# Optimization experiments

Hardware: AMD Instinct MI355X
Metric: run time of the kernel (lower is better)

The kernel has to match this reference:

```python
import jax, jax.numpy as jnp
import numpy as np
import math

STATE_SIZE = 2048
N_TRIPLES = 16_777_216  # number of indexed triples contracted into the scalar sum


def setup_inputs() -> dict:
    key = jax.random.key(0)
    k_in, k_w, k_idx, k_idx_bw = jax.random.split(key, 4)
    stdv = 1.0 / math.sqrt(STATE_SIZE)
    # state vector
    inp = jax.random.normal(k_in, (STATE_SIZE,), dtype=jnp.float32)
    # nn.Parameter(torch.Tensor(3 * state_size ** 2)) with uniform(-stdv, stdv) init
    weights = jax.random.uniform(
        k_w, (3 * STATE_SIZE * STATE_SIZE,), dtype=jnp.float32,
        minval=-stdv, maxval=stdv)
    # triple index list: col 0 indexes weights, cols 1 and 2 index input.
    # indices in [0, STATE_SIZE) are valid for both tensors.
    idxs = jax.random.randint(k_idx, (N_TRIPLES, 3), 0, STATE_SIZE, dtype=jnp.int32)
    # backward bookkeeping indices (inverse lists for the custom CUDA backward);
    # they do not affect the forward math.
    idxs_bw = jax.random.randint(k_idx_bw, (N_TRIPLES, 3), 0, STATE_SIZE, dtype=jnp.int32)
    return {"input": inp, "weights": weights, "idxs": idxs, "idxs_bw": idxs_bw}


def reference(input, weights, idxs, idxs_bw):
    # Indexed tri-linear weighted contraction:
    #   out = sum_m weights[idxs[m,0]] * input[idxs[m,1]] * input[idxs[m,2]]
    w = jnp.take(weights, idxs[:, 0], axis=0)   # [M]
    a = jnp.take(input, idxs[:, 1], axis=0)     # [M]
    b = jnp.take(input, idxs[:, 2], axis=0)     # [M]
    out = jnp.sum(w * a * b)
    return out[None]  # kernel returns outputs[:1] -> shape [1]
```

## Files before the change

kernel.cpp:

```cpp
#include <hip/hip_runtime.h>

#define STATE 2048
#define BLOCK 256
#define GRID  2048

__global__ void trisum_zero_ws(double* __restrict__ ws) {
    if (blockIdx.x == 0 && threadIdx.x == 0) ws[0] = 0.0;
}

__global__ __launch_bounds__(BLOCK) void trisum_main(
        const float* __restrict__ input,
        const float* __restrict__ weights,
        const int4*  __restrict__ idxs4,
        int ngroups,
        double* __restrict__ ws) {
    __shared__ float s_in[STATE];
    __shared__ float s_w[STATE];
    for (int i = threadIdx.x; i < STATE; i += BLOCK) {
        s_in[i] = input[i];
        s_w[i]  = weights[i];
    }
    __syncthreads();

    float acc = 0.0f;
    const int stride = gridDim.x * blockDim.x;
    for (int g = blockIdx.x * blockDim.x + threadIdx.x; g < ngroups; g += stride) {
        const int4 v0 = idxs4[3 * g + 0];
        const int4 v1 = idxs4[3 * g + 1];
        const int4 v2 = idxs4[3 * g + 2];
        acc += s_w[v0.x] * s_in[v0.y] * s_in[v0.z];
        acc += s_w[v0.w] * s_in[v1.x] * s_in[v1.y];
        acc += s_w[v1.z] * s_in[v1.w] * s_in[v2.x];
        acc += s_w[v2.y] * s_in[v2.z] * s_in[v2.w];
    }

    #pragma unroll
    for (int off = 32; off > 0; off >>= 1)
        acc += __shfl_down(acc, off, 64);

    __shared__ double s_part[BLOCK / 64];
    const int wid  = threadIdx.x >> 6;
    const int lane = threadIdx.x & 63;
    if (lane == 0) s_part[wid] = (double)acc;
    __syncthreads();
    if (threadIdx.x == 0) {
        double b = 0.0;
        #pragma unroll
        for (int w = 0; w < BLOCK / 64; ++w) b += s_part[w];
        atomicAdd(ws, b);
    }
}

__global__ void trisum_finalize(const double* __restrict__ ws, float* __restrict__ out) {
    if (blockIdx.x == 0 && threadIdx.x == 0) out[0] = (float)ws[0];
}

extern "C" void kernel_launch(void* const* d_in, const int* in_sizes, int n_in,
                              void* d_out, int out_size, void* d_ws, size_t ws_size,
                              hipStream_t stream) {
    const float* input   = (const float*)d_in[0];
    const float* weights = (const float*)d_in[1];
    const int*   idxs    = (const int*)d_in[2];

    const int ntriples = in_sizes[2] / 3;
    const int ngroups  = ntriples / 4;

    float*  out = (float*)d_out;
    double* ws  = (double*)d_ws;

    trisum_zero_ws<<<1, 64, 0, stream>>>(ws);
    trisum_main<<<GRID, BLOCK, 0, stream>>>(input, weights,
                                            (const int4*)idxs, ngroups, ws);
    trisum_finalize<<<1, 64, 0, stream>>>(ws, out);
}
```

Measured before the change: 373.5 us.

## Process eight triples per thread and replace atomic with per-block partials reduction

Each thread now loads six int4 vectors per iteration, handling eight triples, with unroll 2 to keep more index loads in flight. The single double atomicAdd and the zero-init kernel are replaced by per-block partial sums written to workspace and reduced in a 256-thread finalize kernel, dropping one launch. The wider per-thread load pattern makes each lane read 96 contiguous bytes, which may hurt coalescing compared to the previous 48-byte stride.

```diff
diff --git a/kernel.cpp b/kernel.cpp
--- a/kernel.cpp
+++ b/kernel.cpp
@@ -4,16 +4,12 @@
 #define BLOCK 256
 #define GRID  2048
 
-__global__ void trisum_zero_ws(double* __restrict__ ws) {
-    if (blockIdx.x == 0 && threadIdx.x == 0) ws[0] = 0.0;
-}
-
 __global__ __launch_bounds__(BLOCK) void trisum_main(
         const float* __restrict__ input,
         const float* __restrict__ weights,
         const int4*  __restrict__ idxs4,
-        int ngroups,
-        double* __restrict__ ws) {
+        int ngroups8,
+        double* __restrict__ partials) {
     __shared__ float s_in[STATE];
     __shared__ float s_w[STATE];
     for (int i = threadIdx.x; i < STATE; i += BLOCK) {
@@ -23,15 +19,23 @@
     __syncthreads();
 
     float acc = 0.0f;
-    const int stride = gridDim.x * blockDim.x;
-    for (int g = blockIdx.x * blockDim.x + threadIdx.x; g < ngroups; g += stride) {
-        const int4 v0 = idxs4[3 * g + 0];
-        const int4 v1 = idxs4[3 * g + 1];
-        const int4 v2 = idxs4[3 * g + 2];
+    const int stride = GRID * BLOCK;
+    #pragma unroll 2
+    for (int g = blockIdx.x * BLOCK + threadIdx.x; g < ngroups8; g += stride) {
+        const int4 v0 = idxs4[6 * g + 0];
+        const int4 v1 = idxs4[6 * g + 1];
+        const int4 v2 = idxs4[6 * g + 2];
+        const int4 v3 = idxs4[6 * g + 3];
+        const int4 v4 = idxs4[6 * g + 4];
+        const int4 v5 = idxs4[6 * g + 5];
         acc += s_w[v0.x] * s_in[v0.y] * s_in[v0.z];
         acc += s_w[v0.w] * s_in[v1.x] * s_in[v1.y];
         acc += s_w[v1.z] * s_in[v1.w] * s_in[v2.x];
         acc += s_w[v2.y] * s_in[v2.z] * s_in[v2.w];
+        acc += s_w[v3.x] * s_in[v3.y] * s_in[v3.z];
+        acc += s_w[v3.w] * s_in[v4.x] * s_in[v4.y];
+        acc += s_w[v4.z] * s_in[v4.w] * s_in[v5.x];
+        acc += s_w[v5.y] * s_in[v5.z] * s_in[v5.w];
     }
 
     #pragma unroll
@@ -39,20 +43,25 @@
         acc += __shfl_down(acc, off, 64);
 
     __shared__ double s_part[BLOCK / 64];
-    const int wid  = threadIdx.x >> 6;
-    const int lane = threadIdx.x & 63;
-    if (lane == 0) s_part[wid] = (double)acc;
+    if ((threadIdx.x & 63) == 0) s_part[threadIdx.x >> 6] = (double)acc;
     __syncthreads();
     if (threadIdx.x == 0) {
-        double b = 0.0;
-        #pragma unroll
-        for (int w = 0; w < BLOCK / 64; ++w) b += s_part[w];
-        atomicAdd(ws, b);
+        partials[blockIdx.x] = s_part[0] + s_part[1] + s_part[2] + s_part[3];
     }
 }
 
-__global__ void trisum_finalize(const double* __restrict__ ws, float* __restrict__ out) {
-    if (blockIdx.x == 0 && threadIdx.x == 0) out[0] = (float)ws[0];
+__global__ __launch_bounds__(256) void trisum_finalize(
+        const double* __restrict__ partials, float* __restrict__ out) {
+    double a = 0.0;
+    for (int i = threadIdx.x; i < GRID; i += 256) a += partials[i];
+    #pragma unroll
+    for (int off = 32; off > 0; off >>= 1)
+        a += __shfl_down(a, off, 64);
+    __shared__ double s_part[4];
+    if ((threadIdx.x & 63) == 0) s_part[threadIdx.x >> 6] = a;
+    __syncthreads();
+    if (threadIdx.x == 0)
+        out[0] = (float)(s_part[0] + s_part[1] + s_part[2] + s_part[3]);
 }
 
 extern "C" void kernel_launch(void* const* d_in, const int* in_sizes, int n_in,
@@ -63,13 +72,12 @@
     const int*   idxs    = (const int*)d_in[2];
 
     const int ntriples = in_sizes[2] / 3;
-    const int ngroups  = ntriples / 4;
+    const int ngroups8 = ntriples / 8;
 
-    float*  out = (float*)d_out;
-    double* ws  = (double*)d_ws;
+    float*  out      = (float*)d_out;
+    double* partials = (double*)d_ws;
 
-    trisum_zero_ws<<<1, 64, 0, stream>>>(ws);
     trisum_main<<<GRID, BLOCK, 0, stream>>>(input, weights,
-                                            (const int4*)idxs, ngroups, ws);
-    trisum_finalize<<<1, 64, 0, stream>>>(ws, out);
+                                            (const int4*)idxs, ngroups8, partials);
+    trisum_finalize<<<1, 256, 0, stream>>>(partials, out);
 }
```

After: 372.8 us. No clear change (-0.2%).
